# Kernel tuning notes

Hardware: AMD Instinct MI355X
Metric: run time of the kernel (lower is better)

## Reference

```python
import jax, jax.numpy as jnp
import numpy as np

N, E, IN_DIM, H, D = 50000, 1600000, 128, 8, 16


def setup_inputs() -> dict:
    key = jax.random.key(0)
    ks = jax.random.split(key, 9)
    s = 1.0 / np.sqrt(IN_DIM)
    return {
        "h": jax.random.normal(ks[0], (N, IN_DIM), dtype=jnp.float32),
        "Wq": jax.random.normal(ks[1], (IN_DIM, H * D), dtype=jnp.float32) * s,
        "bq": jax.random.normal(ks[2], (H * D,), dtype=jnp.float32) * 0.01,
        "Wk": jax.random.normal(ks[3], (IN_DIM, H * D), dtype=jnp.float32) * s,
        "bk": jax.random.normal(ks[4], (H * D,), dtype=jnp.float32) * 0.01,
        "Wv": jax.random.normal(ks[5], (IN_DIM, H * D), dtype=jnp.float32) * s,
        "bv": jax.random.normal(ks[6], (H * D,), dtype=jnp.float32) * 0.01,
        "src": jax.random.randint(ks[7], (E,), 0, N, dtype=jnp.int32),
        "dst": jax.random.randint(ks[8], (E,), 0, N, dtype=jnp.int32),
    }


def reference(h, Wq, bq, Wk, bk, Wv, bv, src, dst):
    n = h.shape[0]
    # node-level projections, reshaped to [N, H, D]
    Q = (h @ Wq + bq).reshape(n, H, D)
    K = (h @ Wk + bk).reshape(n, H, D)
    V = (h @ Wv + bv).reshape(n, H, D)
    # per-edge score: dot(K[src], Q[dst]) / sqrt(D), exp-clamped -> [E, H]
    score = jnp.sum(K[src] * Q[dst], axis=-1) / np.sqrt(D)
    score = jnp.exp(jnp.clip(score, -5.0, 5.0))
    # score-weighted messages scattered into destination nodes
    m = V[src] * score[:, :, None]                    # [E, H, D]
    wV = jax.ops.segment_sum(m, dst, num_segments=n)  # [N, H, D]
    z = jax.ops.segment_sum(score, dst, num_segments=n)  # [N, H]
    h_out = wV / (z[:, :, None] + 1e-6)
    return h_out.reshape(n, H * D)
```

## Files before the change

### kernel.cpp

```cpp
#include <hip/hip_runtime.h>
#include <hip/hip_bf16.h>

#define IN_DIM 128
#define HH 8
#define DD 16
#define HD 128
#define SCAN_B 256
#define CHUNK 8192

#define MT  64
#define KP  136
#define NCH 128

typedef float f32x4 __attribute__((ext_vector_type(4)));
typedef short s16x8 __attribute__((ext_vector_type(8)));

__device__ __forceinline__ int sniff_fp32(const unsigned short* h_raw) {
  int sane = 0;
#pragma unroll
  for (int i = 0; i < 128; i += 2) {
    const unsigned short u = h_raw[i];
    const int expo = (u >> 7) & 0xFF;
    if (expo >= 112 && expo <= 143) sane++;
  }
  return (sane >= 40) ? 0 : 1;
}

__global__ __launch_bounds__(128) void wt_kernel(
    const unsigned short* __restrict__ h_raw,
    const void* __restrict__ Wq, const void* __restrict__ Wk,
    const void* __restrict__ Wv, __hip_bfloat16* __restrict__ Wt,
    int* __restrict__ flag, int* __restrict__ bucket_size) {
  const int isf = sniff_fp32(h_raw);
  const int n = blockIdx.x;
  const int k = threadIdx.x;
  if (n == 0) {
    if (k == 0) *flag = isf;
    for (int j = k; j < 258; j += 128) bucket_size[j] = 0;
  }
  const int mat = n >> 7;
  const int col = n & 127;
  const void* W = (mat == 0) ? Wq : (mat == 1) ? Wk : Wv;
  float v;
  if (isf) v = ((const float*)W)[(size_t)k * HD + col];
  else     v = __bfloat162float(((const __hip_bfloat16*)W)[(size_t)k * HD + col]);
  Wt[(size_t)n * KP + k] = __float2bfloat16(v);
}

__global__ __launch_bounds__(256) void proj_hist_kernel(
    const void* __restrict__ h, const __hip_bfloat16* __restrict__ Wt,
    const void* __restrict__ bq, const void* __restrict__ bk,
    const void* __restrict__ bv,
    float* __restrict__ Qf, __hip_bfloat16* __restrict__ Kb,
    __hip_bfloat16* __restrict__ Vb,
    const int* __restrict__ flag, int n_nodes,
    const int* __restrict__ dst, int* __restrict__ bucket_size, int n_edges,
    int pgrid) {
  __shared__ short Bs[NCH * KP];
  __shared__ short As[MT * KP];

  const int tid = threadIdx.x;

  if (blockIdx.x >= pgrid) {
    int* lh = (int*)Bs;
    const int e0 = (blockIdx.x - pgrid) * CHUNK;
    const int e1 = (e0 + CHUNK < n_edges) ? e0 + CHUNK : n_edges;
    lh[tid] = 0;
    __syncthreads();
    for (int e = e0 + tid; e < e1; e += 256) atomicAdd(&lh[dst[e] >> 8], 1);
    __syncthreads();
    if (lh[tid] > 0) atomicAdd(&bucket_size[tid], lh[tid]);
    return;
  }

  const int node0 = blockIdx.x * MT;
  const int isf = *flag;

#pragma unroll
  for (int j = 0; j < 16; ++j) {
    const int pid = tid + j * 256;
    const int m = pid >> 6;
    const int kk = (pid & 63) * 2;
    const int g = node0 + m;
    unsigned int pack = 0;
    if (g < n_nodes) {
      if (isf) {
        const float2 f2 = *(const float2*)((const float*)h + (size_t)g * HD + kk);
        const __hip_bfloat16 b0 = __float2bfloat16(f2.x);
        const __hip_bfloat16 b1 = __float2bfloat16(f2.y);
        pack = (unsigned int)(*(const unsigned short*)&b0) |
               ((unsigned int)(*(const unsigned short*)&b1) << 16);
      } else {
        pack = *(const unsigned int*)((const __hip_bfloat16*)h +
                                      (size_t)g * HD + kk);
      }
    }
    *(unsigned int*)&As[m * KP + kk] = pack;
  }
  __syncthreads();

  const int wave = tid >> 6;
  const int lane = tid & 63;
  const int l15 = lane & 15;
  const int quad = lane >> 4;

  s16x8 afrag[4];
#pragma unroll
  for (int k4 = 0; k4 < 4; ++k4)
    afrag[k4] = *(const s16x8*)&As[(wave * 16 + l15) * KP + k4 * 32 + quad * 8];

  for (int c = 0; c < 3; ++c) {
    __syncthreads();
    const uint4* gsrc = (const uint4*)(Wt + (size_t)c * NCH * KP);
    for (int j = tid; j < (NCH * KP * 2) / 16; j += 256)
      ((uint4*)Bs)[j] = gsrc[j];
    __syncthreads();

    f32x4 acc[8];
#pragma unroll
    for (int t = 0; t < 8; ++t) acc[t] = (f32x4){0.f, 0.f, 0.f, 0.f};

#pragma unroll
    for (int t = 0; t < 8; ++t) {
#pragma unroll
      for (int k4 = 0; k4 < 4; ++k4) {
        const s16x8 bfrag =
            *(const s16x8*)&Bs[(t * 16 + l15) * KP + k4 * 32 + quad * 8];
        acc[t] = __builtin_amdgcn_mfma_f32_16x16x32_bf16(afrag[k4], bfrag,
                                                         acc[t], 0, 0, 0);
      }
    }

    const void* bp = (c == 0) ? bq : (c == 1) ? bk : bv;
#pragma unroll
    for (int t = 0; t < 8; ++t) {
      const int ncol = t * 16 + l15;
      const float bias = isf ? ((const float*)bp)[ncol]
                             : __bfloat162float(((const __hip_bfloat16*)bp)[ncol]);
#pragma unroll
      for (int r = 0; r < 4; ++r) {
        const int g = node0 + wave * 16 + quad * 4 + r;
        if (g < n_nodes) {
          const float val = acc[t][r] + bias;
          const size_t o = (size_t)g * HD + ncol;
          if (c == 0)      Qf[o] = val;
          else if (c == 1) Kb[o] = __float2bfloat16(val);
          else             Vb[o] = __float2bfloat16(val);
        }
      }
    }
  }
}

__global__ __launch_bounds__(256) void bucket_scan_kernel(
    const int* __restrict__ bucket_size, int* __restrict__ bucket_base,
    int* __restrict__ bucket_cur, int nbuck, int n_edges) {
  __shared__ int sh[256];
  const int t = threadIdx.x;
  const int v = (t < nbuck) ? bucket_size[t] : 0;
  sh[t] = v;
  __syncthreads();
  for (int off = 1; off < 256; off <<= 1) {
    int add = (t >= off) ? sh[t - off] : 0;
    __syncthreads();
    sh[t] += add;
    __syncthreads();
  }
  const int excl = sh[t] - v;
  if (t < nbuck) {
    bucket_base[t] = excl;
    bucket_cur[t] = excl;
  }
  if (t == 0) bucket_base[nbuck] = n_edges;
}

__global__ __launch_bounds__(256) void bucketize_kernel(
    const int* __restrict__ src, const int* __restrict__ dst,
    int* __restrict__ bucket_cur, unsigned int* __restrict__ ebuf,
    int n_edges) {
  __shared__ int lh[256];
  const int t = threadIdx.x;
  const int e0 = blockIdx.x * CHUNK;
  const int e1 = (e0 + CHUNK < n_edges) ? e0 + CHUNK : n_edges;
  lh[t] = 0;
  __syncthreads();
  for (int e = e0 + t; e < e1; e += 256) atomicAdd(&lh[dst[e] >> 8], 1);
  __syncthreads();
  const int cnt_local = lh[t];
  int base = 0;
  if (cnt_local > 0) base = atomicAdd(&bucket_cur[t], cnt_local);
  __syncthreads();
  lh[t] = base;
  __syncthreads();
  for (int e = e0 + t; e < e1; e += 256) {
    const int d = dst[e];
    const int pos = atomicAdd(&lh[d >> 8], 1);
    ebuf[pos] = ((unsigned int)src[e] << 16) | (unsigned int)d;
  }
}

__global__ __launch_bounds__(256) void bucket_csr_kernel(
    const unsigned int* __restrict__ ebuf, const int* __restrict__ bucket_base,
    int* __restrict__ row_ptr, int* __restrict__ edge_src,
    int n_nodes, int nbuck) {
  __shared__ int lc[256];
  __shared__ int sh[256];
  const int b = blockIdx.x;
  const int t = threadIdx.x;
  const int lo = bucket_base[b], hi = bucket_base[b + 1];
  const int nbase = b << 8;

  lc[t] = 0;
  __syncthreads();
  for (int i = lo + t; i < hi; i += 256)
    atomicAdd(&lc[(ebuf[i] & 0xFFFFu) - nbase], 1);
  __syncthreads();

  const int v = lc[t];
  sh[t] = v;
  __syncthreads();
  for (int off = 1; off < 256; off <<= 1) {
    int add = (t >= off) ? sh[t - off] : 0;
    __syncthreads();
    sh[t] += add;
    __syncthreads();
  }
  const int excl = sh[t] - v;

  const int node = nbase + t;
  if (node < n_nodes) row_ptr[node] = lo + excl;
  if (b == nbuck - 1 && t == 255) row_ptr[n_nodes] = hi;

  __syncthreads();
  lc[t] = lo + excl;
  __syncthreads();
  for (int i = lo + t; i < hi; i += 256) {
    const unsigned int pkd = ebuf[i];
    const int pos = atomicAdd(&lc[(pkd & 0xFFFFu) - nbase], 1);
    edge_src[pos] = (int)(pkd >> 16);
  }
}

__global__ __launch_bounds__(256) void hist_kernel(
    const int* __restrict__ dst, int* __restrict__ cnt, int n_edges) {
  const int e = blockIdx.x * blockDim.x + threadIdx.x;
  if (e < n_edges) atomicAdd(&cnt[dst[e]], 1);
}

__global__ __launch_bounds__(256) void scatter_kernel(
    const int* __restrict__ src, const int* __restrict__ dst,
    int* __restrict__ cursor, int* __restrict__ edge_src, int n_edges) {
  const int e = blockIdx.x * blockDim.x + threadIdx.x;
  if (e < n_edges) {
    const int pos = atomicAdd(&cursor[dst[e]], 1);
    edge_src[pos] = src[e];
  }
}

__global__ __launch_bounds__(SCAN_B) void scan1_kernel(
    const int* __restrict__ cnt, int* __restrict__ exs,
    int* __restrict__ bsum, int n) {
  __shared__ int sh[SCAN_B];
  const int t = threadIdx.x;
  const int i = blockIdx.x * SCAN_B + t;
  int v = (i < n) ? cnt[i] : 0;
  sh[t] = v;
  __syncthreads();
  for (int off = 1; off < SCAN_B; off <<= 1) {
    int add = (t >= off) ? sh[t - off] : 0;
    __syncthreads();
    sh[t] += add;
    __syncthreads();
  }
  if (i < n) exs[i] = sh[t] - v;
  if (t == SCAN_B - 1) bsum[blockIdx.x] = sh[t];
}

__global__ __launch_bounds__(SCAN_B) void scan2_kernel(int* __restrict__ bsum,
                                                       int nb) {
  __shared__ int sh[SCAN_B];
  const int t = threadIdx.x;
  if (nb <= SCAN_B) {
    int v = (t < nb) ? bsum[t] : 0;
    sh[t] = v;
    __syncthreads();
    for (int off = 1; off < SCAN_B; off <<= 1) {
      int add = (t >= off) ? sh[t - off] : 0;
      __syncthreads();
      sh[t] += add;
      __syncthreads();
    }
    if (t < nb) bsum[t] = sh[t] - v;
  } else if (t == 0) {
    int run = 0;
    for (int b = 0; b < nb; ++b) { int v = bsum[b]; bsum[b] = run; run += v; }
  }
}

__global__ __launch_bounds__(SCAN_B) void scan3_kernel(
    const int* __restrict__ exs, const int* __restrict__ bsum,
    int* __restrict__ row_ptr, int* __restrict__ cursor, int n, int n_edges) {
  const int i = blockIdx.x * SCAN_B + threadIdx.x;
  if (i < n) {
    const int v = exs[i] + bsum[blockIdx.x];
    row_ptr[i] = v;
    cursor[i] = v;
  }
  if (i == 0) row_ptr[n] = n_edges;
}

__global__ __launch_bounds__(128) void gather_kernel(
    const int* __restrict__ row_ptr, const int* __restrict__ edge_src,
    const float* __restrict__ Qf, const __hip_bfloat16* __restrict__ Kb,
    const __hip_bfloat16* __restrict__ Vb,
    void* __restrict__ out, const int* __restrict__ flag, int n_nodes) {
  __shared__ float2 sc[2][16 * HH];
  __shared__ float zred[16 * HH];

  const int d = blockIdx.x;
  const int tid = threadIdx.x;

  const int eloc = tid >> 3;
  const int hh8  = tid & 7;
  const int hd16 = tid >> 4;

  const int start = row_ptr[d];
  const int deg = row_ptr[d + 1] - start;

  float qreg[16];
  {
    const f32x4* qp = (const f32x4*)(Qf + (size_t)d * HD + hh8 * 16);
#pragma unroll
    for (int j = 0; j < 4; ++j) {
      const f32x4 q4 = qp[j];
      qreg[j * 4 + 0] = q4[0] * 0.25f;
      qreg[j * 4 + 1] = q4[1] * 0.25f;
      qreg[j * 4 + 2] = q4[2] * 0.25f;
      qreg[j * 4 + 3] = q4[3] * 0.25f;
    }
  }

  float accV = 0.0f;
  float zacc = 0.0f;
  const int ngroups = (deg + 15) >> 4;

  for (int g = 0; g < ngroups; ++g) {
    const int buf = g & 1;
    const int ei = g * 16 + eloc;

    float score = 0.0f;
    int s = 0;
    if (ei < deg) {
      s = edge_src[start + ei];
      const uint4* kp = (const uint4*)(Kb + (size_t)s * HD + hh8 * 16);
      unsigned int kw[8];
      *(uint4*)&kw[0] = kp[0];
      *(uint4*)&kw[4] = kp[1];
      float dot = 0.0f;
#pragma unroll
      for (int i = 0; i < 8; ++i) {
        const float klo = __uint_as_float(kw[i] << 16);
        const float khi = __uint_as_float(kw[i] & 0xFFFF0000u);
        dot = fmaf(qreg[2 * i], klo, dot);
        dot = fmaf(qreg[2 * i + 1], khi, dot);
      }
      score = __expf(fminf(fmaxf(dot, -5.0f), 5.0f));
    }
    zacc += score;
    sc[buf][eloc * HH + hh8] = make_float2(score, __int_as_float(s));
    __syncthreads();

    const int rem = deg - g * 16;
    const int lim = (rem < 16) ? rem : 16;
    if (lim == 16) {
#pragma unroll
      for (int e = 0; e < 16; ++e) {
        const float2 pe = sc[buf][e * HH + hd16];
        const int s2 = __float_as_int(pe.y);
        const unsigned short vu =
            *(const unsigned short*)(Vb + (size_t)s2 * HD + tid);
        accV = fmaf(pe.x, __uint_as_float(((unsigned int)vu) << 16), accV);
      }
    } else {
      for (int e = 0; e < lim; ++e) {
        const float2 pe = sc[buf][e * HH + hd16];
        const int s2 = __float_as_int(pe.y);
        const unsigned short vu =
            *(const unsigned short*)(Vb + (size_t)s2 * HD + tid);
        accV = fmaf(pe.x, __uint_as_float(((unsigned int)vu) << 16), accV);
      }
    }
  }

  zred[eloc * HH + hh8] = zacc;
  __syncthreads();
  float aZ = 0.0f;
#pragma unroll
  for (int i = 0; i < 16; ++i) aZ += zred[i * HH + hd16];

  const float r = accV / (aZ + 1e-6f);
  const size_t o = (size_t)d * HD + tid;
  if (*flag) ((float*)out)[o] = r;
  else       ((__hip_bfloat16*)out)[o] = __float2bfloat16(r);
}

extern "C" void kernel_launch(void* const* d_in, const int* in_sizes, int n_in,
                              void* d_out, int out_size, void* d_ws, size_t ws_size,
                              hipStream_t stream) {
  const void* h  = d_in[0];
  const void* Wq = d_in[1];
  const void* bq = d_in[2];
  const void* Wk = d_in[3];
  const void* bk = d_in[4];
  const void* Wv = d_in[5];
  const void* bv = d_in[6];
  const int* src = (const int*)d_in[7];
  const int* dst = (const int*)d_in[8];

  const int n_nodes = in_sizes[0] / IN_DIM;
  const int n_edges = in_sizes[7];
  const int nb = (n_nodes + SCAN_B - 1) / SCAN_B;
  const int nbuck = (n_nodes + 255) >> 8;

  char* p = (char*)d_ws;
  int* flag = (int*)p;                       p += 256;
  float* Qf = (float*)p;                     p += (size_t)n_nodes * HD * 4;
  __hip_bfloat16* Kb = (__hip_bfloat16*)p;   p += (size_t)n_nodes * HD * 2;
  __hip_bfloat16* Vb = (__hip_bfloat16*)p;   p += (size_t)n_nodes * HD * 2;
  __hip_bfloat16* Wt = (__hip_bfloat16*)p;   p += ((size_t)384 * KP * 2 + 255) / 256 * 256;
  int* bucket_size = (int*)p;                p += 258 * 4;
  int* bucket_base = (int*)p;                p += 258 * 4;
  int* bucket_cur = (int*)p;                 p += 258 * 4;
  int* row_ptr = (int*)p;                    p += (size_t)(n_nodes + 1) * 4;
  unsigned int* ebuf = (unsigned int*)p;     p += (size_t)n_edges * 4;
  int* edge_src = (int*)p;                   p += (size_t)n_edges * 4;
  int* cnt = (int*)p;                        p += (size_t)n_nodes * 4;
  int* exs = (int*)p;                        p += (size_t)n_nodes * 4;
  int* bsum = (int*)p;                       p += (size_t)(nb + 1) * 4;
  int* cursor = (int*)p;                     p += (size_t)n_nodes * 4;

  wt_kernel<<<384, 128, 0, stream>>>((const unsigned short*)h, Wq, Wk, Wv, Wt,
                                     flag, bucket_size);

  const int pgrid = (n_nodes + MT - 1) / MT;
  const int nchunk = (n_edges + CHUNK - 1) / CHUNK;

  if (n_nodes <= 65536) {
    proj_hist_kernel<<<pgrid + nchunk, 256, 0, stream>>>(
        h, Wt, bq, bk, bv, Qf, Kb, Vb, flag, n_nodes, dst, bucket_size,
        n_edges, pgrid);
    bucket_scan_kernel<<<1, 256, 0, stream>>>(bucket_size, bucket_base,
                                              bucket_cur, nbuck, n_edges);
    bucketize_kernel<<<nchunk, 256, 0, stream>>>(src, dst, bucket_cur, ebuf,
                                                 n_edges);
    bucket_csr_kernel<<<nbuck, 256, 0, stream>>>(ebuf, bucket_base, row_ptr,
                                                 edge_src, n_nodes, nbuck);
  } else {
    proj_hist_kernel<<<pgrid, 256, 0, stream>>>(
        h, Wt, bq, bk, bv, Qf, Kb, Vb, flag, n_nodes, dst, bucket_size,
        n_edges, pgrid);
    hipMemsetAsync(cnt, 0, (size_t)n_nodes * sizeof(int), stream);
    const int eb = 256;
    const int egrid = (n_edges + eb - 1) / eb;
    hist_kernel<<<egrid, eb, 0, stream>>>(dst, cnt, n_edges);
    scan1_kernel<<<nb, SCAN_B, 0, stream>>>(cnt, exs, bsum, n_nodes);
    scan2_kernel<<<1, SCAN_B, 0, stream>>>(bsum, nb);
    scan3_kernel<<<nb, SCAN_B, 0, stream>>>(exs, bsum, row_ptr, cursor,
                                            n_nodes, n_edges);
    scatter_kernel<<<egrid, eb, 0, stream>>>(src, dst, cursor, edge_src,
                                             n_edges);
  }

  gather_kernel<<<n_nodes, 128, 0, stream>>>(row_ptr, edge_src, Qf, Kb, Vb,
                                             d_out, flag, n_nodes);
}
```

Baseline: 318.7 us.

## Drop LDS staging in projection and store Q as bf16

The projection kernel no longer stages h and the weight tiles in shared memory. It loads MFMA A and B fragments directly from global memory and pads KP down to 128. Q is now stored as bf16 instead of fp32, which halves Q write and read traffic, and the gather kernel unpacks it. This removes syncs and LDS use and should raise occupancy. The risks are uncoalesced or redundant global weight reads and lower Q precision.

```diff
diff --git a/kernel.cpp b/kernel.cpp
--- a/kernel.cpp
+++ b/kernel.cpp
@@ -9,8 +9,7 @@
 #define CHUNK 8192
 
 #define MT  64
-#define KP  136
-#define NCH 128
+#define KP  128
 
 typedef float f32x4 __attribute__((ext_vector_type(4)));
 typedef short s16x8 __attribute__((ext_vector_type(8)));
@@ -51,18 +50,16 @@
     const void* __restrict__ h, const __hip_bfloat16* __restrict__ Wt,
     const void* __restrict__ bq, const void* __restrict__ bk,
     const void* __restrict__ bv,
-    float* __restrict__ Qf, __hip_bfloat16* __restrict__ Kb,
+    __hip_bfloat16* __restrict__ Qb, __hip_bfloat16* __restrict__ Kb,
     __hip_bfloat16* __restrict__ Vb,
     const int* __restrict__ flag, int n_nodes,
     const int* __restrict__ dst, int* __restrict__ bucket_size, int n_edges,
     int pgrid) {
-  __shared__ short Bs[NCH * KP];
-  __shared__ short As[MT * KP];
+  __shared__ int lh[256];
 
   const int tid = threadIdx.x;
 
   if (blockIdx.x >= pgrid) {
-    int* lh = (int*)Bs;
     const int e0 = (blockIdx.x - pgrid) * CHUNK;
     const int e1 = (e0 + CHUNK < n_edges) ? e0 + CHUNK : n_edges;
     lh[tid] = 0;
@@ -75,46 +72,40 @@
 
   const int node0 = blockIdx.x * MT;
   const int isf = *flag;
-
-#pragma unroll
-  for (int j = 0; j < 16; ++j) {
-    const int pid = tid + j * 256;
-    const int m = pid >> 6;
-    const int kk = (pid & 63) * 2;
-    const int g = node0 + m;
-    unsigned int pack = 0;
-    if (g < n_nodes) {
-      if (isf) {
-        const float2 f2 = *(const float2*)((const float*)h + (size_t)g * HD + kk);
-        const __hip_bfloat16 b0 = __float2bfloat16(f2.x);
-        const __hip_bfloat16 b1 = __float2bfloat16(f2.y);
-        pack = (unsigned int)(*(const unsigned short*)&b0) |
-               ((unsigned int)(*(const unsigned short*)&b1) << 16);
-      } else {
-        pack = *(const unsigned int*)((const __hip_bfloat16*)h +
-                                      (size_t)g * HD + kk);
-      }
-    }
-    *(unsigned int*)&As[m * KP + kk] = pack;
-  }
-  __syncthreads();
 
   const int wave = tid >> 6;
   const int lane = tid & 63;
   const int l15 = lane & 15;
   const int quad = lane >> 4;
 
+  const int g = node0 + wave * 16 + l15;
+  const int gs = (g < n_nodes) ? g : (n_nodes - 1);
   s16x8 afrag[4];
-#pragma unroll
-  for (int k4 = 0; k4 < 4; ++k4)
-    afrag[k4] = *(const s16x8*)&As[(wave * 16 + l15) * KP + k4 * 32 + quad * 8];
+  if (isf) {
+    const float* hp = (const float*)h + (size_t)gs * HD;
+#pragma unroll
+    for (int k4 = 0; k4 < 4; ++k4) {
+      const f32x4 a0 = *(const f32x4*)(hp + k4 * 32 + quad * 8);
+      const f32x4 a1 = *(const f32x4*)(hp + k4 * 32 + quad * 8 + 4);
+      s16x8 fr;
+#pragma unroll
+      for (int j = 0; j < 4; ++j) {
+        const __hip_bfloat16 b0 = __float2bfloat16(a0[j]);
+        const __hip_bfloat16 b1 = __float2bfloat16(a1[j]);
+        fr[j] = *(const short*)&b0;
+        fr[4 + j] = *(const short*)&b1;
+      }
+      afrag[k4] = fr;
+    }
+  } else {
+    const __hip_bfloat16* hp = (const __hip_bfloat16*)h + (size_t)gs * HD;
+#pragma unroll
+    for (int k4 = 0; k4 < 4; ++k4)
+      afrag[k4] = *(const s16x8*)(hp + k4 * 32 + quad * 8);
+  }
 
   for (int c = 0; c < 3; ++c) {
-    __syncthreads();
-    const uint4* gsrc = (const uint4*)(Wt + (size_t)c * NCH * KP);
-    for (int j = tid; j < (NCH * KP * 2) / 16; j += 256)
-      ((uint4*)Bs)[j] = gsrc[j];
-    __syncthreads();
+    const __hip_bfloat16* wb = Wt + (size_t)c * 128 * KP;
 
     f32x4 acc[8];
 #pragma unroll
@@ -125,13 +116,14 @@
 #pragma unroll
       for (int k4 = 0; k4 < 4; ++k4) {
         const s16x8 bfrag =
-            *(const s16x8*)&Bs[(t * 16 + l15) * KP + k4 * 32 + quad * 8];
+            *(const s16x8*)(wb + (t * 16 + l15) * KP + k4 * 32 + quad * 8);
         acc[t] = __builtin_amdgcn_mfma_f32_16x16x32_bf16(afrag[k4], bfrag,
                                                          acc[t], 0, 0, 0);
       }
     }
 
     const void* bp = (c == 0) ? bq : (c == 1) ? bk : bv;
+    __hip_bfloat16* outp = (c == 0) ? Qb : (c == 1) ? Kb : Vb;
 #pragma unroll
     for (int t = 0; t < 8; ++t) {
       const int ncol = t * 16 + l15;
@@ -139,14 +131,9 @@
                              : __bfloat162float(((const __hip_bfloat16*)bp)[ncol]);
 #pragma unroll
       for (int r = 0; r < 4; ++r) {
-        const int g = node0 + wave * 16 + quad * 4 + r;
-        if (g < n_nodes) {
-          const float val = acc[t][r] + bias;
-          const size_t o = (size_t)g * HD + ncol;
-          if (c == 0)      Qf[o] = val;
-          else if (c == 1) Kb[o] = __float2bfloat16(val);
-          else             Vb[o] = __float2bfloat16(val);
-        }
+        const int gw = node0 + wave * 16 + quad * 4 + r;
+        if (gw < n_nodes)
+          outp[(size_t)gw * HD + ncol] = __float2bfloat16(acc[t][r] + bias);
       }
     }
   }
@@ -311,7 +298,7 @@
 
 __global__ __launch_bounds__(128) void gather_kernel(
     const int* __restrict__ row_ptr, const int* __restrict__ edge_src,
-    const float* __restrict__ Qf, const __hip_bfloat16* __restrict__ Kb,
+    const __hip_bfloat16* __restrict__ Qb, const __hip_bfloat16* __restrict__ Kb,
     const __hip_bfloat16* __restrict__ Vb,
     void* __restrict__ out, const int* __restrict__ flag, int n_nodes) {
   __shared__ float2 sc[2][16 * HH];
@@ -329,14 +316,14 @@
 
   float qreg[16];
   {
-    const f32x4* qp = (const f32x4*)(Qf + (size_t)d * HD + hh8 * 16);
-#pragma unroll
-    for (int j = 0; j < 4; ++j) {
-      const f32x4 q4 = qp[j];
-      qreg[j * 4 + 0] = q4[0] * 0.25f;
-      qreg[j * 4 + 1] = q4[1] * 0.25f;
-      qreg[j * 4 + 2] = q4[2] * 0.25f;
-      qreg[j * 4 + 3] = q4[3] * 0.25f;
+    const uint4* qp = (const uint4*)(Qb + (size_t)d * HD + hh8 * 16);
+    unsigned int qw[8];
+    *(uint4*)&qw[0] = qp[0];
+    *(uint4*)&qw[4] = qp[1];
+#pragma unroll
+    for (int i = 0; i < 8; ++i) {
+      qreg[2 * i]     = __uint_as_float(qw[i] << 16) * 0.25f;
+      qreg[2 * i + 1] = __uint_as_float(qw[i] & 0xFFFF0000u) * 0.25f;
     }
   }
 
@@ -424,7 +411,7 @@
 
   char* p = (char*)d_ws;
   int* flag = (int*)p;                       p += 256;
-  float* Qf = (float*)p;                     p += (size_t)n_nodes * HD * 4;
+  __hip_bfloat16* Qb = (__hip_bfloat16*)p;   p += (size_t)n_nodes * HD * 2;
   __hip_bfloat16* Kb = (__hip_bfloat16*)p;   p += (size_t)n_nodes * HD * 2;
   __hip_bfloat16* Vb = (__hip_bfloat16*)p;   p += (size_t)n_nodes * HD * 2;
   __hip_bfloat16* Wt = (__hip_bfloat16*)p;   p += ((size_t)384 * KP * 2 + 255) / 256 * 256;
@@ -447,7 +434,7 @@
 
   if (n_nodes <= 65536) {
     proj_hist_kernel<<<pgrid + nchunk, 256, 0, stream>>>(
-        h, Wt, bq, bk, bv, Qf, Kb, Vb, flag, n_nodes, dst, bucket_size,
+        h, Wt, bq, bk, bv, Qb, Kb, Vb, flag, n_nodes, dst, bucket_size,
         n_edges, pgrid);
     bucket_scan_kernel<<<1, 256, 0, stream>>>(bucket_size, bucket_base,
                                               bucket_cur, nbuck, n_edges);
@@ -457,7 +444,7 @@
                                                  edge_src, n_nodes, nbuck);
   } else {
     proj_hist_kernel<<<pgrid, 256, 0, stream>>>(
-        h, Wt, bq, bk, bv, Qf, Kb, Vb, flag, n_nodes, dst, bucket_size,
+        h, Wt, bq, bk, bv, Qb, Kb, Vb, flag, n_nodes, dst, bucket_size,
         n_edges, pgrid);
     hipMemsetAsync(cnt, 0, (size_t)n_nodes * sizeof(int), stream);
     const int eb = 256;
@@ -471,6 +458,6 @@
                                              n_edges);
   }
 
-  gather_kernel<<<n_nodes, 128, 0, stream>>>(row_ptr, edge_src, Qf, Kb, Vb,
+  gather_kernel<<<n_nodes, 128, 0, stream>>>(row_ptr, edge_src, Qb, Kb, Vb,
                                              d_out, flag, n_nodes);
 }
```

Result: slower. 325.1 us (+2.0%).

## Fuse bucket scan into histogram via last-block pattern, store Q as bf16, register-cache bucketize

Applied to the files above, without the earlier changes.

Removes the separate bucket_scan kernel launch: the last histogram block to finish, detected with an atomic counter, performs the bucket prefix scan itself. Histogram blocks now come first in the grid so they are scheduled early. Q is stored in bf16 instead of fp32, which halves Q write and read traffic at some cost in precision. Bucketize uses smaller chunks and keeps the packed src/dst words in registers, so dst and src are read only once. The completion counter in bucket_size[256] relies on wt_kernel zeroing it each call.

```diff
diff --git a/kernel.cpp b/kernel.cpp
--- a/kernel.cpp
+++ b/kernel.cpp
@@ -7,6 +7,7 @@
 #define HD 128
 #define SCAN_B 256
 #define CHUNK 8192
+#define CHUNK2 2048
 
 #define MT  64
 #define KP  136
@@ -51,29 +52,55 @@
     const void* __restrict__ h, const __hip_bfloat16* __restrict__ Wt,
     const void* __restrict__ bq, const void* __restrict__ bk,
     const void* __restrict__ bv,
-    float* __restrict__ Qf, __hip_bfloat16* __restrict__ Kb,
+    __hip_bfloat16* __restrict__ Qb, __hip_bfloat16* __restrict__ Kb,
     __hip_bfloat16* __restrict__ Vb,
     const int* __restrict__ flag, int n_nodes,
-    const int* __restrict__ dst, int* __restrict__ bucket_size, int n_edges,
-    int pgrid) {
+    const int* __restrict__ dst, int* __restrict__ bucket_size,
+    int* __restrict__ bucket_base, int* __restrict__ bucket_cur,
+    int n_edges, int nchunk, int nbuck) {
   __shared__ short Bs[NCH * KP];
   __shared__ short As[MT * KP];
+  __shared__ int is_last;
 
   const int tid = threadIdx.x;
 
-  if (blockIdx.x >= pgrid) {
+  if (blockIdx.x < nchunk) {
     int* lh = (int*)Bs;
-    const int e0 = (blockIdx.x - pgrid) * CHUNK;
+    int* shs = (int*)As;
+    const int e0 = blockIdx.x * CHUNK;
     const int e1 = (e0 + CHUNK < n_edges) ? e0 + CHUNK : n_edges;
     lh[tid] = 0;
     __syncthreads();
     for (int e = e0 + tid; e < e1; e += 256) atomicAdd(&lh[dst[e] >> 8], 1);
     __syncthreads();
     if (lh[tid] > 0) atomicAdd(&bucket_size[tid], lh[tid]);
+    __threadfence();
+    if (tid == 0) {
+      const int old = atomicAdd(&bucket_size[256], 1);
+      is_last = (old == nchunk - 1);
+    }
+    __syncthreads();
+    if (!is_last) return;
+
+    const int v = (tid < nbuck) ? atomicAdd(&bucket_size[tid], 0) : 0;
+    shs[tid] = v;
+    __syncthreads();
+    for (int off = 1; off < 256; off <<= 1) {
+      int add = (tid >= off) ? shs[tid - off] : 0;
+      __syncthreads();
+      shs[tid] += add;
+      __syncthreads();
+    }
+    const int excl = shs[tid] - v;
+    if (tid < nbuck) {
+      bucket_base[tid] = excl;
+      bucket_cur[tid] = excl;
+    }
+    if (tid == 0) bucket_base[nbuck] = n_edges;
     return;
   }
 
-  const int node0 = blockIdx.x * MT;
+  const int node0 = (blockIdx.x - nchunk) * MT;
   const int isf = *flag;
 
 #pragma unroll
@@ -132,6 +159,7 @@
     }
 
     const void* bp = (c == 0) ? bq : (c == 1) ? bk : bv;
+    __hip_bfloat16* outp = (c == 0) ? Qb : (c == 1) ? Kb : Vb;
 #pragma unroll
     for (int t = 0; t < 8; ++t) {
       const int ncol = t * 16 + l15;
@@ -140,38 +168,11 @@
 #pragma unroll
       for (int r = 0; r < 4; ++r) {
         const int g = node0 + wave * 16 + quad * 4 + r;
-        if (g < n_nodes) {
-          const float val = acc[t][r] + bias;
-          const size_t o = (size_t)g * HD + ncol;
-          if (c == 0)      Qf[o] = val;
-          else if (c == 1) Kb[o] = __float2bfloat16(val);
-          else             Vb[o] = __float2bfloat16(val);
-        }
-      }
-    }
-  }
-}
-
-__global__ __launch_bounds__(256) void bucket_scan_kernel(
-    const int* __restrict__ bucket_size, int* __restrict__ bucket_base,
-    int* __restrict__ bucket_cur, int nbuck, int n_edges) {
-  __shared__ int sh[256];
-  const int t = threadIdx.x;
-  const int v = (t < nbuck) ? bucket_size[t] : 0;
-  sh[t] = v;
-  __syncthreads();
-  for (int off = 1; off < 256; off <<= 1) {
-    int add = (t >= off) ? sh[t - off] : 0;
-    __syncthreads();
-    sh[t] += add;
-    __syncthreads();
-  }
-  const int excl = sh[t] - v;
-  if (t < nbuck) {
-    bucket_base[t] = excl;
-    bucket_cur[t] = excl;
-  }
-  if (t == 0) bucket_base[nbuck] = n_edges;
+        if (g < n_nodes)
+          outp[(size_t)g * HD + ncol] = __float2bfloat16(acc[t][r] + bias);
+      }
+    }
+  }
 }
 
 __global__ __launch_bounds__(256) void bucketize_kernel(
@@ -180,11 +181,20 @@
     int n_edges) {
   __shared__ int lh[256];
   const int t = threadIdx.x;
-  const int e0 = blockIdx.x * CHUNK;
-  const int e1 = (e0 + CHUNK < n_edges) ? e0 + CHUNK : n_edges;
+  const int e0 = blockIdx.x * CHUNK2;
+  const int e1 = (e0 + CHUNK2 < n_edges) ? e0 + CHUNK2 : n_edges;
   lh[t] = 0;
   __syncthreads();
-  for (int e = e0 + t; e < e1; e += 256) atomicAdd(&lh[dst[e] >> 8], 1);
+  unsigned int pk[CHUNK2 / 256];
+#pragma unroll
+  for (int j = 0; j < CHUNK2 / 256; ++j) {
+    const int e = e0 + j * 256 + t;
+    if (e < e1) {
+      const int d = dst[e];
+      pk[j] = ((unsigned int)src[e] << 16) | (unsigned int)d;
+      atomicAdd(&lh[d >> 8], 1);
+    }
+  }
   __syncthreads();
   const int cnt_local = lh[t];
   int base = 0;
@@ -192,10 +202,13 @@
   __syncthreads();
   lh[t] = base;
   __syncthreads();
-  for (int e = e0 + t; e < e1; e += 256) {
-    const int d = dst[e];
-    const int pos = atomicAdd(&lh[d >> 8], 1);
-    ebuf[pos] = ((unsigned int)src[e] << 16) | (unsigned int)d;
+#pragma unroll
+  for (int j = 0; j < CHUNK2 / 256; ++j) {
+    const int e = e0 + j * 256 + t;
+    if (e < e1) {
+      const int pos = atomicAdd(&lh[(pk[j] & 0xFFFFu) >> 8], 1);
+      ebuf[pos] = pk[j];
+    }
   }
 }
 
@@ -311,7 +324,7 @@
 
 __global__ __launch_bounds__(128) void gather_kernel(
     const int* __restrict__ row_ptr, const int* __restrict__ edge_src,
-    const float* __restrict__ Qf, const __hip_bfloat16* __restrict__ Kb,
+    const __hip_bfloat16* __restrict__ Qb, const __hip_bfloat16* __restrict__ Kb,
     const __hip_bfloat16* __restrict__ Vb,
     void* __restrict__ out, const int* __restrict__ flag, int n_nodes) {
   __shared__ float2 sc[2][16 * HH];
@@ -329,14 +342,14 @@
 
   float qreg[16];
   {
-    const f32x4* qp = (const f32x4*)(Qf + (size_t)d * HD + hh8 * 16);
-#pragma unroll
-    for (int j = 0; j < 4; ++j) {
-      const f32x4 q4 = qp[j];
-      qreg[j * 4 + 0] = q4[0] * 0.25f;
-      qreg[j * 4 + 1] = q4[1] * 0.25f;
-      qreg[j * 4 + 2] = q4[2] * 0.25f;
-      qreg[j * 4 + 3] = q4[3] * 0.25f;
+    const uint4* qp = (const uint4*)(Qb + (size_t)d * HD + hh8 * 16);
+    unsigned int qw[8];
+    *(uint4*)&qw[0] = qp[0];
+    *(uint4*)&qw[4] = qp[1];
+#pragma unroll
+    for (int i = 0; i < 8; ++i) {
+      qreg[2 * i]     = __uint_as_float(qw[i] << 16) * 0.25f;
+      qreg[2 * i + 1] = __uint_as_float(qw[i] & 0xFFFF0000u) * 0.25f;
     }
   }
 
@@ -424,7 +437,7 @@
 
   char* p = (char*)d_ws;
   int* flag = (int*)p;                       p += 256;
-  float* Qf = (float*)p;                     p += (size_t)n_nodes * HD * 4;
+  __hip_bfloat16* Qb = (__hip_bfloat16*)p;   p += (size_t)n_nodes * HD * 2;
   __hip_bfloat16* Kb = (__hip_bfloat16*)p;   p += (size_t)n_nodes * HD * 2;
   __hip_bfloat16* Vb = (__hip_bfloat16*)p;   p += (size_t)n_nodes * HD * 2;
   __hip_bfloat16* Wt = (__hip_bfloat16*)p;   p += ((size_t)384 * KP * 2 + 255) / 256 * 256;
@@ -446,19 +459,18 @@
   const int nchunk = (n_edges + CHUNK - 1) / CHUNK;
 
   if (n_nodes <= 65536) {
-    proj_hist_kernel<<<pgrid + nchunk, 256, 0, stream>>>(
-        h, Wt, bq, bk, bv, Qf, Kb, Vb, flag, n_nodes, dst, bucket_size,
-        n_edges, pgrid);
-    bucket_scan_kernel<<<1, 256, 0, stream>>>(bucket_size, bucket_base,
-                                              bucket_cur, nbuck, n_edges);
-    bucketize_kernel<<<nchunk, 256, 0, stream>>>(src, dst, bucket_cur, ebuf,
-                                                 n_edges);
+    proj_hist_kernel<<<nchunk + pgrid, 256, 0, stream>>>(
+        h, Wt, bq, bk, bv, Qb, Kb, Vb, flag, n_nodes, dst, bucket_size,
+        bucket_base, bucket_cur, n_edges, nchunk, nbuck);
+    const int nchunk2 = (n_edges + CHUNK2 - 1) / CHUNK2;
+    bucketize_kernel<<<nchunk2, 256, 0, stream>>>(src, dst, bucket_cur, ebuf,
+                                                  n_edges);
     bucket_csr_kernel<<<nbuck, 256, 0, stream>>>(ebuf, bucket_base, row_ptr,
                                                  edge_src, n_nodes, nbuck);
   } else {
     proj_hist_kernel<<<pgrid, 256, 0, stream>>>(
-        h, Wt, bq, bk, bv, Qf, Kb, Vb, flag, n_nodes, dst, bucket_size,
-        n_edges, pgrid);
+        h, Wt, bq, bk, bv, Qb, Kb, Vb, flag, n_nodes, dst, bucket_size,
+        bucket_base, bucket_cur, n_edges, 0, nbuck);
     hipMemsetAsync(cnt, 0, (size_t)n_nodes * sizeof(int), stream);
     const int eb = 256;
     const int egrid = (n_edges + eb - 1) / eb;
@@ -471,6 +483,6 @@
                                              n_edges);
   }
 
-  gather_kernel<<<n_nodes, 128, 0, stream>>>(row_ptr, edge_src, Qf, Kb, Vb,
+  gather_kernel<<<n_nodes, 128, 0, stream>>>(row_ptr, edge_src, Qb, Kb, Vb,
                                              d_out, flag, n_nodes);
 }
```

Result: slower. 335.3 us (+5.2%).
